# Performance work log

Measured on AMD Instinct MI355X. Metric: run time of the kernel, lower is better.

The kernel has to match this reference:

```python
import jax, jax.numpy as jnp
import numpy as np

B, N, D = 16, 256, 1152
HR = 1.0
H = int(N * HR)              # token-mixer hidden dim = 256
TOP_K = int(3 * D**2 / (2 * HR * N**2 + 10 * D))  # = 27
TOP_K = max(1, TOP_K)
E = 10 * TOP_K               # 270 experts
MLP_H = int(D * 4.0)


def gelu_tanh(x):
    return jax.nn.gelu(x, approximate=True)


def setup_inputs() -> dict:
    key = jax.random.key(0)
    ks = jax.random.split(key, 16)
    s = 0.02
    return {
        "x": jax.random.normal(ks[0], (B, N, D), jnp.float32),
        "c": jax.random.normal(ks[1], (B, D), jnp.float32),
        "router_w": jax.random.normal(ks[2], (E, D), jnp.float32) * s,
        "fc1_w": jax.random.normal(ks[3], (E, H, N), jnp.float32) * s,
        "fc1_b": jnp.zeros((E, H), jnp.float32),
        "fc2_w": jax.random.normal(ks[4], (E, N, H), jnp.float32) * s,
        "fc2_b": jnp.zeros((E, N), jnp.float32),
        "out_proj_w": jax.random.normal(ks[5], (D, D), jnp.float32) * s,
        "out_proj_b": jnp.zeros((D,), jnp.float32),
        "adaln_w": jax.random.normal(ks[6], (6 * D, D), jnp.float32) * s,
        "adaln_b": jnp.zeros((6 * D,), jnp.float32),
        "mlp_w1": jax.random.normal(ks[7], (MLP_H, D), jnp.float32) * s,
        "mlp_b1": jnp.zeros((MLP_H,), jnp.float32),
        "mlp_w2": jax.random.normal(ks[8], (D, MLP_H), jnp.float32) * s,
        "mlp_b2": jnp.zeros((D,), jnp.float32),
    }


def _forward(x, c, router_w, fc1_w, fc1_b, fc2_w, fc2_b,
             out_proj_w, out_proj_b, adaln_w, adaln_b,
             mlp_w1, mlp_b1, mlp_w2, mlp_b2):
    # adaLN modulation: SiLU -> Linear(D, 6D) -> chunk 6
    mod = jax.nn.silu(c) @ adaln_w.T + adaln_b                      # [B, 6D]
    sh_mom, sc_mom, g_mom, sh_mlp, sc_mlp, g_mlp = jnp.split(mod, 6, axis=1)
    modx = x * (1.0 + sc_mom[:, None, :]) + sh_mom[:, None, :]      # [B,N,D]

    # ---- Mixture of Mixers ----
    router_logits = modx.mean(axis=1) @ router_w.T                  # [B,E]
    probs = jax.nn.softmax(router_logits, axis=-1)
    topk_w, topk_idx = jax.lax.top_k(probs, TOP_K)                  # [B,K]
    topk_w = topk_w / topk_w.sum(axis=-1, keepdims=True)

    # TokenMixer layernorm: normalize across token axis (dim=1), eps 1e-5, no affine
    mu = modx.mean(axis=1, keepdims=True)
    var = modx.var(axis=1, keepdims=True)
    z = (modx - mu) * jax.lax.rsqrt(var + 1e-5)                     # [B,N,D]

    # Gather selected expert weights and apply token-mixing MLP per slot
    w1 = fc1_w[topk_idx]                                            # [B,K,H,N]
    b1 = fc1_b[topk_idx]                                            # [B,K,H]
    w2 = fc2_w[topk_idx]                                            # [B,K,N,H]
    b2 = fc2_b[topk_idx]                                            # [B,K,N]
    h = jnp.einsum('bkhn,bnd->bkhd', w1, z) + b1[..., None]         # [B,K,H,D]
    h = gelu_tanh(h)
    o = jnp.einsum('bknh,bkhd->bknd', w2, h) + b2[..., None]        # [B,K,N,D]
    mom = jnp.einsum('bk,bknd->bnd', topk_w, o)                     # [B,N,D]
    mom_out = mom @ out_proj_w.T + out_proj_b

    # load-balancing aux loss (top-1 routing fraction)
    top1 = topk_idx[:, 0]
    frac = jax.nn.one_hot(top1, E, dtype=probs.dtype).mean(axis=0)  # [E]
    aux_loss = E * jnp.sum(probs.mean(axis=0) * frac)

    x = x + g_mom[:, None, :] * mom_out

    # norm2: LN over last dim, eps 1e-6, no affine
    mu2 = x.mean(axis=-1, keepdims=True)
    var2 = x.var(axis=-1, keepdims=True)
    n2 = (x - mu2) * jax.lax.rsqrt(var2 + 1e-6)
    m = n2 * (1.0 + sc_mlp[:, None, :]) + sh_mlp[:, None, :]
    mlp = gelu_tanh(m @ mlp_w1.T + mlp_b1) @ mlp_w2.T + mlp_b2
    x = x + g_mlp[:, None, :] * mlp
    return x, aux_loss


def reference(x, c, router_w, fc1_w, fc1_b, fc2_w, fc2_b,
              out_proj_w, out_proj_b, adaln_w, adaln_b,
              mlp_w1, mlp_b1, mlp_w2, mlp_b2):
    return _forward(x, c, router_w, fc1_w, fc1_b, fc2_w, fc2_b,
                    out_proj_w, out_proj_b, adaln_w, adaln_b,
                    mlp_w1, mlp_b1, mlp_w2, mlp_b2)
```

## Files before the change

kernel.cpp:

```cpp
#include <hip/hip_runtime.h>
#include <stdint.h>


#define B_ 16
#define N_ 256
#define D_ 1152
#define E_ 270
#define KTOP 27
#define MLPH 4608
#define D6 6912

typedef float f32;
typedef unsigned short u16;
typedef unsigned int u32;

typedef __attribute__((ext_vector_type(8))) short bf16x8;
typedef __attribute__((ext_vector_type(4))) float f32x4;

__device__ __forceinline__ u16 f2b(f32 x){
  union{f32 f;u32 u;} v; v.f=x;
  u32 r=v.u+0x7FFFu+((v.u>>16)&1u);
  return (u16)(r>>16);
}
__device__ __forceinline__ u32 f2b2(f32 a,f32 b){ return (u32)f2b(a)|((u32)f2b(b)<<16); }
__device__ __forceinline__ f32 gelu_t(f32 x){
  f32 u=0.7978845608028654f*(x+0.044715f*x*x*x);
  f32 e=__expf(2.0f*u);
  return 0.5f*x*(2.0f-2.0f/(e+1.0f));
}
__device__ __forceinline__ f32x4 mfma16(bf16x8 a,bf16x8 b,f32x4 c){
  return __builtin_amdgcn_mfma_f32_16x16x32_bf16(a,b,c,0,0,0);
}

__global__ void k_modinit(f32* __restrict__ mod, const f32* __restrict__ adb){
  int i=blockIdx.x*256+threadIdx.x;
  mod[i]=adb[i%D6];
}
__global__ void k_adaln(f32* __restrict__ mod, const f32* __restrict__ c, const f32* __restrict__ aw){
  __shared__ f32 scs[B_][128];
  const int tid=threadIdx.x;
  const int d0=blockIdx.y*128;
  for(int i=tid;i<B_*128;i+=256){
    int b=i>>7,d=i&127;
    f32 v=c[b*D_+d0+d];
    scs[b][d]=v/(1.f+__expf(-v));
  }
  __syncthreads();
  const int j=blockIdx.x*256+tid;
  f32 acc[B_];
  #pragma unroll
  for(int b=0;b<B_;b++) acc[b]=0.f;
  const f32* wr=aw+(size_t)j*D_+d0;
  for(int d=0;d<128;d+=4){
    float4 w4=*(const float4*)(wr+d);
    #pragma unroll
    for(int b=0;b<B_;b++)
      acc[b]+=w4.x*scs[b][d]+w4.y*scs[b][d+1]+w4.z*scs[b][d+2]+w4.w*scs[b][d+3];
  }
  #pragma unroll
  for(int b=0;b<B_;b++) atomicAdd(&mod[b*D6+j],acc[b]);
}

__global__ void k_colstats(f32* __restrict__ mu, f32* __restrict__ rstd,
                           const f32* __restrict__ x, const f32* __restrict__ mod){
  const int d=(blockIdx.x*64+threadIdx.x)*2;
  const int b=blockIdx.y;
  const f32* xp=x+(size_t)b*N_*D_+d;
  f32 s1a=0,s1b=0,s2a=0,s2b=0;
  for(int n=0;n<N_;n++){
    float2 v=*(const float2*)(xp+(size_t)n*D_);
    s1a+=v.x; s1b+=v.y; s2a+=v.x*v.x; s2b+=v.y*v.y;
  }
  #pragma unroll
  for(int q=0;q<2;q++){
    f32 s1=q?s1b:s1a, s2=q?s2b:s2a;
    int dd=d+q;
    f32 xb=s1*(1.f/N_);
    f32 vx=s2*(1.f/N_)-xb*xb;
    f32 a=1.f+mod[b*D6+D_+dd];
    f32 m=xb*a+mod[b*D6+dd];
    mu[b*D_+dd]=m;
    rstd[b*D_+dd]=rsqrtf(vx*a*a+1e-5f);
  }
}

__global__ void k_ztrans(u16* __restrict__ zt, const f32* __restrict__ x,
                         const f32* __restrict__ mu, const f32* __restrict__ rstd,
                         const f32* __restrict__ mod){
  __shared__ f32 xs[64][129];
  const int tid=threadIdx.x;
  const int dt0=blockIdx.x*128, n0=blockIdx.y*64, b=blockIdx.z;
  const f32* xp=x+((size_t)b*N_+n0)*D_+dt0;
  for(int s=tid;s<2048;s+=256){
    int n=s>>5, cq=(s&31)*4;
    float4 v=*(const float4*)(xp+(size_t)n*D_+cq);
    xs[n][cq]=v.x; xs[n][cq+1]=v.y; xs[n][cq+2]=v.z; xs[n][cq+3]=v.w;
  }
  __syncthreads();
  for(int s=tid;s<1024;s+=256){
    int d=s>>3, g=s&7;
    int gd=dt0+d;
    f32 a=1.f+mod[b*D6+D_+gd];
    f32 sh=mod[b*D6+gd];
    f32 m=mu[b*D_+gd], rs=rstd[b*D_+gd];
    f32 z[8];
    #pragma unroll
    for(int i=0;i<8;i++) z[i]=(xs[g*8+i][d]*a+sh-m)*rs;
    uint4 o; o.x=f2b2(z[0],z[1]); o.y=f2b2(z[2],z[3]); o.z=f2b2(z[4],z[5]); o.w=f2b2(z[6],z[7]);
    *(uint4*)(zt+((size_t)b*D_+gd)*N_+n0+g*8)=o;
  }
}

__global__ void k_router(f32* __restrict__ logits, const f32* __restrict__ mu, const f32* __restrict__ rw){
  const int e=blockIdx.x, lane=threadIdx.x;
  f32 acc[B_];
  #pragma unroll
  for(int b=0;b<B_;b++) acc[b]=0.f;
  const f32* wr=rw+(size_t)e*D_;
  for(int i=0;i<9;i++){
    const int d=(lane+i*64)*2;
    const float2 w2=*(const float2*)(wr+d);
    #pragma unroll
    for(int b=0;b<B_;b++){
      const float2 m2=*(const float2*)(mu+b*D_+d);
      acc[b]+=w2.x*m2.x+w2.y*m2.y;
    }
  }
  #pragma unroll
  for(int b=0;b<B_;b++){
    f32 v=acc[b];
    #pragma unroll
    for(int off=32;off;off>>=1) v+=__shfl_xor(v,off);
    if(lane==0) logits[b*E_+e]=v;
  }
}

__global__ void k_topk(int* __restrict__ tki, f32* __restrict__ tkw, f32* __restrict__ bias_n,
                       f32* __restrict__ aux_out, const f32* __restrict__ logits,
                       const f32* __restrict__ b2){
  __shared__ f32 probs[B_][E_];
  __shared__ int top1[B_];
  const int tid=threadIdx.x, b=tid>>6, lane=tid&63;
  f32 p[5];
  f32 mx=-1e30f;
  #pragma unroll
  for(int i=0;i<5;i++){ int e=lane+i*64; p[i]=(e<E_)?logits[b*E_+e]:-1e30f; mx=fmaxf(mx,p[i]); }
  #pragma unroll
  for(int off=32;off;off>>=1) mx=fmaxf(mx,__shfl_xor(mx,off));
  f32 sum=0;
  #pragma unroll
  for(int i=0;i<5;i++){ int e=lane+i*64; if(e<E_){ p[i]=__expf(p[i]-mx); sum+=p[i]; } else p[i]=-1.f; }
  #pragma unroll
  for(int off=32;off;off>>=1) sum+=__shfl_xor(sum,off);
  const f32 inv=1.f/sum;
  #pragma unroll
  for(int i=0;i<5;i++){ int e=lane+i*64; if(e<E_){ p[i]*=inv; probs[b][e]=p[i]; } }
  int sidx[KTOP]; f32 sp[KTOP]; f32 swsum=0;
  for(int k=0;k<KTOP;k++){
    f32 bv=-2.f; int bi=E_;
    #pragma unroll
    for(int i=0;i<5;i++){ int e=lane+i*64; if(p[i]>bv||(p[i]==bv&&e<bi)){bv=p[i];bi=e;} }
    #pragma unroll
    for(int off=32;off;off>>=1){
      f32 ov=__shfl_xor(bv,off); int oi=__shfl_xor(bi,off);
      if(ov>bv||(ov==bv&&oi<bi)){bv=ov;bi=oi;}
    }
    sidx[k]=bi; sp[k]=bv; swsum+=bv;
    #pragma unroll
    for(int i=0;i<5;i++){ int e=lane+i*64; if(e==bi) p[i]=-1.f; }
  }
  if(lane==0){
    top1[b]=sidx[0];
    for(int k=0;k<KTOP;k++){ tki[b*KTOP+k]=sidx[k]; tkw[b*KTOP+k]=sp[k]/swsum; }
  }
  f32 accn[4]={0,0,0,0};
  for(int k=0;k<KTOP;k++){
    const f32* br=b2+(size_t)sidx[k]*N_;
    const f32 w=sp[k]/swsum;
    #pragma unroll
    for(int j=0;j<4;j++) accn[j]+=w*br[lane+j*64];
  }
  #pragma unroll
  for(int j=0;j<4;j++) bias_n[b*N_+lane+j*64]=accn[j];
  __syncthreads();
  if(tid<64){
    f32 s=0;
    for(int pr=tid;pr<256;pr+=64) s+=probs[pr&15][top1[pr>>4]];
    #pragma unroll
    for(int off=32;off;off>>=1) s+=__shfl_xor(s,off);
    if(tid==0) aux_out[0]=s*((f32)E_/(f32)(B_*B_));
  }
}

__global__ void k_wconv(u16* __restrict__ dst, const f32* __restrict__ src){
  const size_t i=((size_t)blockIdx.x*256+threadIdx.x)*8;
  float4 a=*(const float4*)(src+i), b4=*(const float4*)(src+i+4);
  uint4 o; o.x=f2b2(a.x,a.y); o.y=f2b2(a.z,a.w); o.z=f2b2(b4.x,b4.y); o.w=f2b2(b4.z,b4.w);
  *(uint4*)(dst+i)=o;
}

__global__ __launch_bounds__(512,2) void k_expert(
  f32* __restrict__ mom, const u16* __restrict__ w1b, const u16* __restrict__ w2b,
  const u16* __restrict__ zt, const int* __restrict__ tki, const f32* __restrict__ tkw,
  const f32* __restrict__ fc1b){
  __shared__ u16 wc[2][256][40];
  __shared__ u16 zc[2][128][40];
  __shared__ u16 hlds[128][264];
  __shared__ f32 b1s[256];
  const int tid=threadIdx.x, lane=tid&63, wave=tid>>6;
  const int dt0=blockIdx.x*128, b=blockIdx.z, k0=blockIdx.y*9;
  const int row0=wave*32, c16=lane&15, r4=((lane>>4)<<2), kof=((lane>>4)<<3);
  const int wr0=tid>>2, wq=tid&3;
  const int zr=tid>>2, zq=tid&3;
  f32x4 macc[2][8];
  #pragma unroll
  for(int i=0;i<2;i++)
    #pragma unroll
    for(int j=0;j<8;j++) macc[i][j]=(f32x4){0.f,0.f,0.f,0.f};
  const u16* ztb=zt+((size_t)b*D_+dt0)*N_;
  uint4 rw0,rw1,rz;
  for(int kk=0;kk<9;kk++){
    const int e=tki[b*KTOP+k0+kk];
    const f32 wk=tkw[b*KTOP+k0+kk];
    const u16* W1=w1b+(size_t)e*65536;
    const u16* W2=w2b+(size_t)e*65536;
    if(tid<256) b1s[tid]=fc1b[e*256+tid];
    f32x4 hacc[2][8];
    #pragma unroll
    for(int i=0;i<2;i++)
      #pragma unroll
      for(int j=0;j<8;j++) hacc[i][j]=(f32x4){0.f,0.f,0.f,0.f};
    rw0=*(const uint4*)(W1+(size_t)wr0*256+wq*8);
    rw1=*(const uint4*)(W1+(size_t)(wr0+128)*256+wq*8);
    rz =*(const uint4*)(ztb+(size_t)zr*256+zq*8);
    *(uint4*)&wc[0][wr0][wq*8]=rw0;
    *(uint4*)&wc[0][wr0+128][wq*8]=rw1;
    *(uint4*)&zc[0][zr][zq*8]=rz;
    __syncthreads();
    #pragma unroll 1
    for(int kc=0;kc<8;kc++){
      if(kc<7){
        rw0=*(const uint4*)(W1+(size_t)wr0*256+(kc+1)*32+wq*8);
        rw1=*(const uint4*)(W1+(size_t)(wr0+128)*256+(kc+1)*32+wq*8);
        rz =*(const uint4*)(ztb+(size_t)zr*256+(kc+1)*32+zq*8);
      }
      {
        const int bi=kc&1;
        bf16x8 af0=*(const bf16x8*)&wc[bi][row0+c16][kof];
        bf16x8 af1=*(const bf16x8*)&wc[bi][row0+16+c16][kof];
        #pragma unroll
        for(int ct=0;ct<8;ct++){
          bf16x8 bfr=*(const bf16x8*)&zc[bi][ct*16+c16][kof];
          hacc[0][ct]=mfma16(af0,bfr,hacc[0][ct]);
          hacc[1][ct]=mfma16(af1,bfr,hacc[1][ct]);
        }
      }
      if(kc<7){
        const int bi=(kc+1)&1;
        *(uint4*)&wc[bi][wr0][wq*8]=rw0;
        *(uint4*)&wc[bi][wr0+128][wq*8]=rw1;
        *(uint4*)&zc[bi][zr][zq*8]=rz;
      }
      __syncthreads();
    }
    #pragma unroll
    for(int rt=0;rt<2;rt++){
      const int hr=row0+rt*16+r4;
      #pragma unroll
      for(int ct=0;ct<8;ct++){
        const int dcol=ct*16+c16;
        f32 v0=gelu_t(hacc[rt][ct][0]+b1s[hr+0])*wk;
        f32 v1=gelu_t(hacc[rt][ct][1]+b1s[hr+1])*wk;
        f32 v2=gelu_t(hacc[rt][ct][2]+b1s[hr+2])*wk;
        f32 v3=gelu_t(hacc[rt][ct][3]+b1s[hr+3])*wk;
        uint2 o; o.x=f2b2(v0,v1); o.y=f2b2(v2,v3);
        *(uint2*)&hlds[dcol][hr]=o;
      }
    }
    rw0=*(const uint4*)(W2+(size_t)wr0*256+wq*8);
    rw1=*(const uint4*)(W2+(size_t)(wr0+128)*256+wq*8);
    *(uint4*)&wc[0][wr0][wq*8]=rw0;
    *(uint4*)&wc[0][wr0+128][wq*8]=rw1;
    __syncthreads();
    #pragma unroll 1
    for(int kc=0;kc<8;kc++){
      if(kc<7){
        rw0=*(const uint4*)(W2+(size_t)wr0*256+(kc+1)*32+wq*8);
        rw1=*(const uint4*)(W2+(size_t)(wr0+128)*256+(kc+1)*32+wq*8);
      }
      {
        const int bi=kc&1;
        bf16x8 af0=*(const bf16x8*)&wc[bi][row0+c16][kof];
        bf16x8 af1=*(const bf16x8*)&wc[bi][row0+16+c16][kof];
        #pragma unroll
        for(int ct=0;ct<8;ct++){
          bf16x8 bfr=*(const bf16x8*)&hlds[ct*16+c16][kc*32+kof];
          macc[0][ct]=mfma16(af0,bfr,macc[0][ct]);
          macc[1][ct]=mfma16(af1,bfr,macc[1][ct]);
        }
      }
      if(kc<7){
        const int bi=(kc+1)&1;
        *(uint4*)&wc[bi][wr0][wq*8]=rw0;
        *(uint4*)&wc[bi][wr0+128][wq*8]=rw1;
      }
      __syncthreads();
    }
  }
  f32* mb=mom+(size_t)b*N_*D_+dt0;
  #pragma unroll
  for(int rt=0;rt<2;rt++){
    const int nr=row0+rt*16+r4;
    #pragma unroll
    for(int ct=0;ct<8;ct++){
      const int dc=ct*16+c16;
      #pragma unroll
      for(int j=0;j<4;j++)
        atomicAdd(&mb[(size_t)(nr+j)*D_+dc],macc[rt][ct][j]);
    }
  }
}

__global__ void k_momcomb(u16* __restrict__ mb, const f32* __restrict__ mom, const f32* __restrict__ bias_n){
  const size_t i=((size_t)blockIdx.x*256+threadIdx.x)*4;
  const int t=(int)(i/D_);
  float4 a=*(const float4*)(mom+i);
  const f32 bn=bias_n[t];
  uint2 o; o.x=f2b2(a.x+bn,a.y+bn); o.y=f2b2(a.z+bn,a.w+bn);
  *(uint2*)(mb+i)=o;
}

template<int EPI>
__global__ __launch_bounds__(256,2) void k_gemm(
  const u16* __restrict__ A, const f32* __restrict__ Wf, const f32* __restrict__ bias,
  const f32* __restrict__ aux1, const f32* __restrict__ mod,
  f32* __restrict__ outf, u16* __restrict__ outb, const int K, const int ldo){
  __shared__ u16 asb[2][128][72];
  __shared__ u16 wsb[2][128][72];
  const int tid=threadIdx.x, lane=tid&63, wave=tid>>6;
  const int nt0=blockIdx.x*128, mt0=blockIdx.y*128;
  const int row0=wave*32, c16=lane&15, r4=((lane>>4)<<2), kof=((lane>>4)<<3);
  f32x4 acc[2][8];
  #pragma unroll
  for(int i=0;i<2;i++)
    #pragma unroll
    for(int j=0;j<8;j++) acc[i][j]=(f32x4){0.f,0.f,0.f,0.f};
  const int NK=K>>6;
  uint4 ra[4]; float4 rwv[8];
  auto ldA=[&](int kc){
    #pragma unroll
    for(int s=0;s<4;s++){ int slot=tid+s*256; int row=slot>>3,q=slot&7;
      ra[s]=*(const uint4*)(A+(size_t)(mt0+row)*K+(size_t)kc*64+q*8); } };
  auto stA=[&](int bi){
    #pragma unroll
    for(int s=0;s<4;s++){ int slot=tid+s*256; int row=slot>>3,q=slot&7;
      *(uint4*)&asb[bi][row][q*8]=ra[s]; } };
  auto ldW=[&](int kc){
    #pragma unroll
    for(int s=0;s<4;s++){ int slot=tid+s*256; int row=slot>>3,q=slot&7;
      const f32* p=Wf+(size_t)(nt0+row)*K+(size_t)kc*64+q*8;
      rwv[2*s]=*(const float4*)p; rwv[2*s+1]=*(const float4*)(p+4); } };
  auto stW=[&](int bi){
    #pragma unroll
    for(int s=0;s<4;s++){ int slot=tid+s*256; int row=slot>>3,q=slot&7;
      uint4 o; o.x=f2b2(rwv[2*s].x,rwv[2*s].y); o.y=f2b2(rwv[2*s].z,rwv[2*s].w);
      o.z=f2b2(rwv[2*s+1].x,rwv[2*s+1].y); o.w=f2b2(rwv[2*s+1].z,rwv[2*s+1].w);
      *(uint4*)&wsb[bi][row][q*8]=o; } };
  ldA(0); ldW(0); stA(0); stW(0);
  __syncthreads();
  #pragma unroll 1
  for(int kc=0;kc<NK;kc++){
    if(kc+1<NK){ ldA(kc+1); ldW(kc+1); }
    {
      const int bi=kc&1;
      #pragma unroll
      for(int ks=0;ks<2;ks++){
        bf16x8 af0=*(const bf16x8*)&asb[bi][row0+c16][ks*32+kof];
        bf16x8 af1=*(const bf16x8*)&asb[bi][row0+16+c16][ks*32+kof];
        #pragma unroll
        for(int ct=0;ct<8;ct++){
          bf16x8 bfr=*(const bf16x8*)&wsb[bi][ct*16+c16][ks*32+kof];
          acc[0][ct]=mfma16(af0,bfr,acc[0][ct]);
          acc[1][ct]=mfma16(af1,bfr,acc[1][ct]);
        }
      }
    }
    if(kc+1<NK){ stA((kc+1)&1); stW((kc+1)&1); }
    __syncthreads();
  }
  #pragma unroll
  for(int rt=0;rt<2;rt++){
    #pragma unroll
    for(int ct=0;ct<8;ct++){
      const int cc=nt0+ct*16+c16;
      const f32 bv=bias[cc];
      #pragma unroll
      for(int j=0;j<4;j++){
        const int r=mt0+row0+rt*16+r4+j;
        f32 v=acc[rt][ct][j]+bv;
        if constexpr(EPI==1){
          f32 g=mod[(r>>8)*D6+2*D_+cc];
          outf[(size_t)r*ldo+cc]=aux1[(size_t)r*ldo+cc]+g*v;
        } else if constexpr(EPI==2){
          outb[(size_t)r*ldo+cc]=f2b(gelu_t(v));
        } else {
          f32 g=mod[(r>>8)*D6+5*D_+cc];
          outf[(size_t)r*ldo+cc]=aux1[(size_t)r*D_+cc]+g*v;
        }
      }
    }
  }
}

__global__ void k_ln2(f32* __restrict__ st, const f32* __restrict__ y){
  const int t=blockIdx.x, tid=threadIdx.x;
  f32 s1=0,s2=0;
  for(int i=tid;i<D_;i+=128){ f32 v=y[(size_t)t*D_+i]; s1+=v; s2+=v*v; }
  #pragma unroll
  for(int off=32;off;off>>=1){ s1+=__shfl_xor(s1,off); s2+=__shfl_xor(s2,off); }
  __shared__ f32 r1[2],r2[2];
  if((tid&63)==0){ r1[tid>>6]=s1; r2[tid>>6]=s2; }
  __syncthreads();
  if(tid==0){
    f32 a=r1[0]+r1[1], q=r2[0]+r2[1];
    f32 m=a*(1.0f/D_);
    f32 var=q*(1.0f/D_)-m*m;
    st[t*2]=m; st[t*2+1]=rsqrtf(var+1e-6f);
  }
}

__global__ void k_mnorm(u16* __restrict__ mb, const f32* __restrict__ y,
                        const f32* __restrict__ st, const f32* __restrict__ mod){
  const size_t i=((size_t)blockIdx.x*256+threadIdx.x)*4;
  const int t=(int)(i/D_); const int b=t>>8; const int d=(int)(i-(size_t)t*D_);
  float4 v=*(const float4*)(y+i);
  const f32 m=st[t*2], rs=st[t*2+1];
  float4 sc=*(const float4*)(mod+b*D6+4*D_+d);
  float4 sh=*(const float4*)(mod+b*D6+3*D_+d);
  f32 a0=(v.x-m)*rs*(1.f+sc.x)+sh.x;
  f32 a1=(v.y-m)*rs*(1.f+sc.y)+sh.y;
  f32 a2=(v.z-m)*rs*(1.f+sc.z)+sh.z;
  f32 a3=(v.w-m)*rs*(1.f+sc.w)+sh.w;
  uint2 o; o.x=f2b2(a0,a1); o.y=f2b2(a2,a3);
  *(uint2*)(mb+i)=o;
}

extern "C" void kernel_launch(void* const* d_in, const int* in_sizes, int n_in,
                              void* d_out, int out_size, void* d_ws, size_t ws_size,
                              hipStream_t stream){
  const f32* x  =(const f32*)d_in[0];
  const f32* c  =(const f32*)d_in[1];
  const f32* rw =(const f32*)d_in[2];
  const f32* f1w=(const f32*)d_in[3];
  const f32* f1b=(const f32*)d_in[4];
  const f32* f2w=(const f32*)d_in[5];
  const f32* f2b_=(const f32*)d_in[6];
  const f32* opw=(const f32*)d_in[7];
  const f32* opb=(const f32*)d_in[8];
  const f32* adw=(const f32*)d_in[9];
  const f32* adb=(const f32*)d_in[10];
  const f32* m1w=(const f32*)d_in[11];
  const f32* m1b=(const f32*)d_in[12];
  const f32* m2w=(const f32*)d_in[13];
  const f32* m2b=(const f32*)d_in[14];
  f32* out=(f32*)d_out;

  char* wsp=(char*)d_ws; size_t off=0;
  auto alloc=[&](size_t bytes)->void*{ void* p=wsp+off; off=(off+bytes+255)&~(size_t)255; return p; };
  f32* mod   =(f32*)alloc((size_t)B_*D6*4);
  f32* mu    =(f32*)alloc((size_t)B_*D_*4);
  f32* rstd  =(f32*)alloc((size_t)B_*D_*4);
  f32* logits=(f32*)alloc((size_t)B_*E_*4);
  int* tki   =(int*)alloc((size_t)B_*KTOP*4);
  f32* tkw   =(f32*)alloc((size_t)B_*KTOP*4);
  f32* bias_n=(f32*)alloc((size_t)B_*N_*4);
  f32* ln2st =(f32*)alloc((size_t)B_*N_*2*4);
  u16* mom_b =(u16*)alloc((size_t)B_*N_*D_*2);
  u16* zt    =(u16*)alloc((size_t)B_*N_*D_*2);
  u16* w1b   =(u16*)alloc((size_t)E_*65536*2);
  u16* w2b   =(u16*)alloc((size_t)E_*65536*2);
  f32* mom=out;
  f32* y  =out;
  u16* m_b=zt;
  u16* t_b=w1b;
  f32* aux_out=out+(size_t)B_*N_*D_;

  hipMemsetAsync(mom,0,(size_t)B_*N_*D_*4,stream);
  k_modinit<<<432,256,0,stream>>>(mod,adb);
  k_adaln<<<dim3(27,9),256,0,stream>>>(mod,c,adw);
  k_colstats<<<dim3(9,16),64,0,stream>>>(mu,rstd,x,mod);
  k_ztrans<<<dim3(9,4,16),256,0,stream>>>(zt,x,mu,rstd,mod);
  k_router<<<E_,64,0,stream>>>(logits,mu,rw);
  k_topk<<<1,1024,0,stream>>>(tki,tkw,bias_n,aux_out,logits,f2b_);
  k_wconv<<<8640,256,0,stream>>>(w1b,f1w);
  k_wconv<<<8640,256,0,stream>>>(w2b,f2w);
  k_expert<<<dim3(9,3,16),512,0,stream>>>(mom,w1b,w2b,zt,tki,tkw,f1b);
  k_momcomb<<<4608,256,0,stream>>>(mom_b,mom,bias_n);
  k_gemm<1><<<dim3(9,32),256,0,stream>>>(mom_b,opw,opb,x,mod,y,nullptr,D_,D_);
  k_ln2<<<4096,128,0,stream>>>(ln2st,y);
  k_mnorm<<<4608,256,0,stream>>>(m_b,y,ln2st,mod);
  k_gemm<2><<<dim3(36,32),256,0,stream>>>(m_b,m1w,m1b,nullptr,nullptr,nullptr,t_b,D_,MLPH);
  k_gemm<3><<<dim3(9,32),256,0,stream>>>(t_b,m2w,m2b,y,mod,out,nullptr,MLPH,D_);
}
```

Baseline: 1.127 ms.

## Retile expert kernel, pre-convert dense weights to bf16, add grid swizzle

The expert kernel is restructured to split the hidden dimension into two 128-row halves. fc1 and fc2 now run as two smaller GEMM stages that reuse the z tile's LDS for the hidden activations. Smaller LDS lets occupancy rise to 4 blocks, and the grid is flattened with an 8-way swizzle. The dense GEMMs now read bf16 weights that are pre-converted once by extra k_wconv launches, instead of converting fp32 in the inner loop. They also gain an M-tile template (64 rows for the D-output GEMMs) and the same block swizzle. The trade-offs are extra conversion passes and more synchronisation points in the expert kernel.

New measurement: 1.579 ms. +40.1%, slower.

```diff
diff --git a/kernel.cpp b/kernel.cpp
--- a/kernel.cpp
+++ b/kernel.cpp
@@ -105,7 +105,7 @@
     f32 m=mu[b*D_+gd], rs=rstd[b*D_+gd];
     f32 z[8];
     #pragma unroll
-    for(int i=0;i<8;i++) z[i]=(xs[g*8+i][d]*a+sh-m)*rs;
+    for(int i2=0;i2<8;i2++) z[i2]=(xs[g*8+i2][d]*a+sh-m)*rs;
     uint4 o; o.x=f2b2(z[0],z[1]); o.y=f2b2(z[2],z[3]); o.z=f2b2(z[4],z[5]); o.w=f2b2(z[6],z[7]);
     *(uint4*)(zt+((size_t)b*D_+gd)*N_+n0+g*8)=o;
   }
@@ -199,124 +199,121 @@
   *(uint4*)(dst+i)=o;
 }
 
-__global__ __launch_bounds__(512,2) void k_expert(
+__global__ __launch_bounds__(512,4) void k_expert(
   f32* __restrict__ mom, const u16* __restrict__ w1b, const u16* __restrict__ w2b,
   const u16* __restrict__ zt, const int* __restrict__ tki, const f32* __restrict__ tkw,
   const f32* __restrict__ fc1b){
-  __shared__ u16 wc[2][256][40];
-  __shared__ u16 zc[2][128][40];
-  __shared__ u16 hlds[128][264];
+  __shared__ __align__(16) u16 wc[2][128][72];
+  __shared__ __align__(16) u16 zc[2][128][72];
   __shared__ f32 b1s[256];
+  u16 (*hlds)[136]=reinterpret_cast<u16 (*)[136]>(&zc[0][0][0]);
+  const int bid=blockIdx.x;
+  const int g8=bid&7, jj=bid>>3;
+  const int xb=jj%9, ghi=jj/9;
+  const int g=ghi*8+g8;
+  const int b=g/3, ks=g%3;
+  const int dt0=xb*128;
   const int tid=threadIdx.x, lane=tid&63, wave=tid>>6;
-  const int dt0=blockIdx.x*128, b=blockIdx.z, k0=blockIdx.y*9;
-  const int row0=wave*32, c16=lane&15, r4=((lane>>4)<<2), kof=((lane>>4)<<3);
-  const int wr0=tid>>2, wq=tid&3;
-  const int zr=tid>>2, zq=tid&3;
-  f32x4 macc[2][8];
+  const int c16=lane&15, r4=(lane>>4)<<2, kof=(lane>>4)<<3;
+  const int srow=tid>>2, sq=(tid&3)<<4;
+  f32x4 acc2[2][8];
   #pragma unroll
   for(int i=0;i<2;i++)
     #pragma unroll
-    for(int j=0;j<8;j++) macc[i][j]=(f32x4){0.f,0.f,0.f,0.f};
+    for(int j=0;j<8;j++) acc2[i][j]=(f32x4){0.f,0.f,0.f,0.f};
   const u16* ztb=zt+((size_t)b*D_+dt0)*N_;
-  uint4 rw0,rw1,rz;
   for(int kk=0;kk<9;kk++){
-    const int e=tki[b*KTOP+k0+kk];
-    const f32 wk=tkw[b*KTOP+k0+kk];
-    const u16* W1=w1b+(size_t)e*65536;
-    const u16* W2=w2b+(size_t)e*65536;
+    const int e=tki[b*KTOP+ks*9+kk];
+    const f32 wk=tkw[b*KTOP+ks*9+kk];
     if(tid<256) b1s[tid]=fc1b[e*256+tid];
-    f32x4 hacc[2][8];
-    #pragma unroll
-    for(int i=0;i<2;i++)
+    uint4 a0,a1,z0,z1;
+    #pragma unroll 1
+    for(int hh=0;hh<2;hh++){
+      const u16* W1h=w1b+(size_t)e*65536+hh*128*256;
+      f32x4 acc1[8];
       #pragma unroll
-      for(int j=0;j<8;j++) hacc[i][j]=(f32x4){0.f,0.f,0.f,0.f};
-    rw0=*(const uint4*)(W1+(size_t)wr0*256+wq*8);
-    rw1=*(const uint4*)(W1+(size_t)(wr0+128)*256+wq*8);
-    rz =*(const uint4*)(ztb+(size_t)zr*256+zq*8);
-    *(uint4*)&wc[0][wr0][wq*8]=rw0;
-    *(uint4*)&wc[0][wr0+128][wq*8]=rw1;
-    *(uint4*)&zc[0][zr][zq*8]=rz;
-    __syncthreads();
-    #pragma unroll 1
-    for(int kc=0;kc<8;kc++){
-      if(kc<7){
-        rw0=*(const uint4*)(W1+(size_t)wr0*256+(kc+1)*32+wq*8);
-        rw1=*(const uint4*)(W1+(size_t)(wr0+128)*256+(kc+1)*32+wq*8);
-        rz =*(const uint4*)(ztb+(size_t)zr*256+(kc+1)*32+zq*8);
+      for(int j=0;j<8;j++) acc1[j]=(f32x4){0.f,0.f,0.f,0.f};
+      a0=*(const uint4*)(W1h+srow*256+sq);   a1=*(const uint4*)(W1h+srow*256+sq+8);
+      z0=*(const uint4*)(ztb+(size_t)srow*256+sq); z1=*(const uint4*)(ztb+(size_t)srow*256+sq+8);
+      *(uint4*)&wc[0][srow][sq]=a0; *(uint4*)&wc[0][srow][sq+8]=a1;
+      *(uint4*)&zc[0][srow][sq]=z0; *(uint4*)&zc[0][srow][sq+8]=z1;
+      __syncthreads();
+      #pragma unroll 1
+      for(int kc=0;kc<4;kc++){
+        if(kc<3){
+          const int co=(kc+1)*64+sq;
+          a0=*(const uint4*)(W1h+srow*256+co);   a1=*(const uint4*)(W1h+srow*256+co+8);
+          z0=*(const uint4*)(ztb+(size_t)srow*256+co); z1=*(const uint4*)(ztb+(size_t)srow*256+co+8);
+        }
+        const int bi=kc&1;
+        #pragma unroll
+        for(int k2=0;k2<2;k2++){
+          bf16x8 af=*(const bf16x8*)&wc[bi][wave*16+c16][k2*32+kof];
+          #pragma unroll
+          for(int ct=0;ct<8;ct++){
+            bf16x8 bf=*(const bf16x8*)&zc[bi][ct*16+c16][k2*32+kof];
+            acc1[ct]=mfma16(af,bf,acc1[ct]);
+          }
+        }
+        if(kc<3){
+          const int nb=(kc+1)&1;
+          *(uint4*)&wc[nb][srow][sq]=a0; *(uint4*)&wc[nb][srow][sq+8]=a1;
+          *(uint4*)&zc[nb][srow][sq]=z0; *(uint4*)&zc[nb][srow][sq+8]=z1;
+        }
+        __syncthreads();
       }
-      {
-        const int bi=kc&1;
-        bf16x8 af0=*(const bf16x8*)&wc[bi][row0+c16][kof];
-        bf16x8 af1=*(const bf16x8*)&wc[bi][row0+16+c16][kof];
-        #pragma unroll
-        for(int ct=0;ct<8;ct++){
-          bf16x8 bfr=*(const bf16x8*)&zc[bi][ct*16+c16][kof];
-          hacc[0][ct]=mfma16(af0,bfr,hacc[0][ct]);
-          hacc[1][ct]=mfma16(af1,bfr,hacc[1][ct]);
+      f32 bb[4];
+      #pragma unroll
+      for(int j=0;j<4;j++) bb[j]=b1s[hh*128+wave*16+r4+j];
+      #pragma unroll
+      for(int ct=0;ct<8;ct++){
+        f32 v0=gelu_t(acc1[ct][0]+bb[0])*wk;
+        f32 v1=gelu_t(acc1[ct][1]+bb[1])*wk;
+        f32 v2=gelu_t(acc1[ct][2]+bb[2])*wk;
+        f32 v3=gelu_t(acc1[ct][3]+bb[3])*wk;
+        uint2 o; o.x=f2b2(v0,v1); o.y=f2b2(v2,v3);
+        *(uint2*)&hlds[ct*16+c16][wave*16+r4]=o;
+      }
+      __syncthreads();
+      #pragma unroll 1
+      for(int nh=0;nh<2;nh++){
+        const u16* W2h=w2b+(size_t)e*65536+nh*128*256+hh*128;
+        a0=*(const uint4*)(W2h+srow*256+sq); a1=*(const uint4*)(W2h+srow*256+sq+8);
+        *(uint4*)&wc[0][srow][sq]=a0; *(uint4*)&wc[0][srow][sq+8]=a1;
+        __syncthreads();
+        #pragma unroll 1
+        for(int kc=0;kc<2;kc++){
+          if(kc<1){
+            a0=*(const uint4*)(W2h+srow*256+64+sq); a1=*(const uint4*)(W2h+srow*256+64+sq+8);
+          }
+          const int bi=kc&1;
+          #pragma unroll
+          for(int k2=0;k2<2;k2++){
+            bf16x8 af=*(const bf16x8*)&wc[bi][wave*16+c16][k2*32+kof];
+            #pragma unroll
+            for(int ct=0;ct<8;ct++){
+              bf16x8 bf=*(const bf16x8*)&hlds[ct*16+c16][kc*64+k2*32+kof];
+              acc2[nh][ct]=mfma16(af,bf,acc2[nh][ct]);
+            }
+          }
+          if(kc<1){
+            *(uint4*)&wc[1][srow][sq]=a0; *(uint4*)&wc[1][srow][sq+8]=a1;
+          }
+          __syncthreads();
         }
       }
-      if(kc<7){
-        const int bi=(kc+1)&1;
-        *(uint4*)&wc[bi][wr0][wq*8]=rw0;
-        *(uint4*)&wc[bi][wr0+128][wq*8]=rw1;
-        *(uint4*)&zc[bi][zr][zq*8]=rz;
-      }
-      __syncthreads();
     }
-    #pragma unroll
-    for(int rt=0;rt<2;rt++){
-      const int hr=row0+rt*16+r4;
-      #pragma unroll
-      for(int ct=0;ct<8;ct++){
-        const int dcol=ct*16+c16;
-        f32 v0=gelu_t(hacc[rt][ct][0]+b1s[hr+0])*wk;
-        f32 v1=gelu_t(hacc[rt][ct][1]+b1s[hr+1])*wk;
-        f32 v2=gelu_t(hacc[rt][ct][2]+b1s[hr+2])*wk;
-        f32 v3=gelu_t(hacc[rt][ct][3]+b1s[hr+3])*wk;
-        uint2 o; o.x=f2b2(v0,v1); o.y=f2b2(v2,v3);
-        *(uint2*)&hlds[dcol][hr]=o;
-      }
-    }
-    rw0=*(const uint4*)(W2+(size_t)wr0*256+wq*8);
-    rw1=*(const uint4*)(W2+(size_t)(wr0+128)*256+wq*8);
-    *(uint4*)&wc[0][wr0][wq*8]=rw0;
-    *(uint4*)&wc[0][wr0+128][wq*8]=rw1;
-    __syncthreads();
-    #pragma unroll 1
-    for(int kc=0;kc<8;kc++){
-      if(kc<7){
-        rw0=*(const uint4*)(W2+(size_t)wr0*256+(kc+1)*32+wq*8);
-        rw1=*(const uint4*)(W2+(size_t)(wr0+128)*256+(kc+1)*32+wq*8);
-      }
-      {
-        const int bi=kc&1;
-        bf16x8 af0=*(const bf16x8*)&wc[bi][row0+c16][kof];
-        bf16x8 af1=*(const bf16x8*)&wc[bi][row0+16+c16][kof];
-        #pragma unroll
-        for(int ct=0;ct<8;ct++){
-          bf16x8 bfr=*(const bf16x8*)&hlds[ct*16+c16][kc*32+kof];
-          macc[0][ct]=mfma16(af0,bfr,macc[0][ct]);
-          macc[1][ct]=mfma16(af1,bfr,macc[1][ct]);
-        }
-      }
-      if(kc<7){
-        const int bi=(kc+1)&1;
-        *(uint4*)&wc[bi][wr0][wq*8]=rw0;
-        *(uint4*)&wc[bi][wr0+128][wq*8]=rw1;
-      }
-      __syncthreads();
-    }
   }
   f32* mb=mom+(size_t)b*N_*D_+dt0;
   #pragma unroll
-  for(int rt=0;rt<2;rt++){
-    const int nr=row0+rt*16+r4;
+  for(int nh=0;nh<2;nh++){
+    const int nr=nh*128+wave*16+r4;
     #pragma unroll
     for(int ct=0;ct<8;ct++){
       const int dc=ct*16+c16;
       #pragma unroll
       for(int j=0;j<4;j++)
-        atomicAdd(&mb[(size_t)(nr+j)*D_+dc],macc[rt][ct][j]);
+        atomicAdd(&mb[(size_t)(nr+j)*D_+dc],acc2[nh][ct][j]);
     }
   }
 }
@@ -330,42 +327,45 @@
   *(uint2*)(mb+i)=o;
 }
 
-template<int EPI>
+template<int MT,int EPI>
 __global__ __launch_bounds__(256,2) void k_gemm(
-  const u16* __restrict__ A, const f32* __restrict__ Wf, const f32* __restrict__ bias,
+  const u16* __restrict__ A, const u16* __restrict__ W, const f32* __restrict__ bias,
   const f32* __restrict__ aux1, const f32* __restrict__ mod,
   f32* __restrict__ outf, u16* __restrict__ outb, const int K, const int ldo){
-  __shared__ u16 asb[2][128][72];
-  __shared__ u16 wsb[2][128][72];
+  constexpr int RT=MT/64;
+  constexpr int AN=MT/32;
+  __shared__ __align__(16) u16 asb[2][MT][72];
+  __shared__ __align__(16) u16 wsb[2][128][72];
+  const int lin=blockIdx.x+gridDim.x*blockIdx.y;
+  const int y8=lin&7, t2=lin>>3;
+  const int xb=t2%gridDim.x, yhi=t2/gridDim.x;
+  const int yb=yhi*8+y8;
+  const int nt0=xb*128, mt0=yb*MT;
   const int tid=threadIdx.x, lane=tid&63, wave=tid>>6;
-  const int nt0=blockIdx.x*128, mt0=blockIdx.y*128;
-  const int row0=wave*32, c16=lane&15, r4=((lane>>4)<<2), kof=((lane>>4)<<3);
-  f32x4 acc[2][8];
-  #pragma unroll
-  for(int i=0;i<2;i++)
+  const int c16=lane&15, r4=(lane>>4)<<2, kof=(lane>>4)<<3;
+  const int row0=wave*16*RT;
+  const int wrow=tid>>1, wq=(tid&1)<<5;
+  const int arow=(MT==128)?(tid>>1):(tid>>2);
+  const int aq  =(MT==128)?((tid&1)<<5):((tid&3)<<4);
+  f32x4 acc[RT][8];
+  #pragma unroll
+  for(int i=0;i<RT;i++)
     #pragma unroll
     for(int j=0;j<8;j++) acc[i][j]=(f32x4){0.f,0.f,0.f,0.f};
   const int NK=K>>6;
-  uint4 ra[4]; float4 rwv[8];
+  uint4 ra[AN], rw[4];
   auto ldA=[&](int kc){
     #pragma unroll
-    for(int s=0;s<4;s++){ int slot=tid+s*256; int row=slot>>3,q=slot&7;
-      ra[s]=*(const uint4*)(A+(size_t)(mt0+row)*K+(size_t)kc*64+q*8); } };
+    for(int s=0;s<AN;s++) ra[s]=*(const uint4*)(A+(size_t)(mt0+arow)*K+kc*64+aq+s*8); };
   auto stA=[&](int bi){
     #pragma unroll
-    for(int s=0;s<4;s++){ int slot=tid+s*256; int row=slot>>3,q=slot&7;
-      *(uint4*)&asb[bi][row][q*8]=ra[s]; } };
+    for(int s=0;s<AN;s++) *(uint4*)&asb[bi][arow][aq+s*8]=ra[s]; };
   auto ldW=[&](int kc){
     #pragma unroll
-    for(int s=0;s<4;s++){ int slot=tid+s*256; int row=slot>>3,q=slot&7;
-      const f32* p=Wf+(size_t)(nt0+row)*K+(size_t)kc*64+q*8;
-      rwv[2*s]=*(const float4*)p; rwv[2*s+1]=*(const float4*)(p+4); } };
+    for(int s=0;s<4;s++) rw[s]=*(const uint4*)(W+(size_t)(nt0+wrow)*K+kc*64+wq+s*8); };
   auto stW=[&](int bi){
     #pragma unroll
-    for(int s=0;s<4;s++){ int slot=tid+s*256; int row=slot>>3,q=slot&7;
-      uint4 o; o.x=f2b2(rwv[2*s].x,rwv[2*s].y); o.y=f2b2(rwv[2*s].z,rwv[2*s].w);
-      o.z=f2b2(rwv[2*s+1].x,rwv[2*s+1].y); o.w=f2b2(rwv[2*s+1].z,rwv[2*s+1].w);
-      *(uint4*)&wsb[bi][row][q*8]=o; } };
+    for(int s=0;s<4;s++) *(uint4*)&wsb[bi][wrow][wq+s*8]=rw[s]; };
   ldA(0); ldW(0); stA(0); stW(0);
   __syncthreads();
   #pragma unroll 1
@@ -374,14 +374,15 @@
     {
       const int bi=kc&1;
       #pragma unroll
-      for(int ks=0;ks<2;ks++){
-        bf16x8 af0=*(const bf16x8*)&asb[bi][row0+c16][ks*32+kof];
-        bf16x8 af1=*(const bf16x8*)&asb[bi][row0+16+c16][ks*32+kof];
+      for(int k2=0;k2<2;k2++){
         #pragma unroll
-        for(int ct=0;ct<8;ct++){
-          bf16x8 bfr=*(const bf16x8*)&wsb[bi][ct*16+c16][ks*32+kof];
-          acc[0][ct]=mfma16(af0,bfr,acc[0][ct]);
-          acc[1][ct]=mfma16(af1,bfr,acc[1][ct]);
+        for(int rt=0;rt<RT;rt++){
+          bf16x8 af=*(const bf16x8*)&asb[bi][row0+rt*16+c16][k2*32+kof];
+          #pragma unroll
+          for(int ct=0;ct<8;ct++){
+            bf16x8 bf=*(const bf16x8*)&wsb[bi][ct*16+c16][k2*32+kof];
+            acc[rt][ct]=mfma16(af,bf,acc[rt][ct]);
+          }
         }
       }
     }
@@ -389,7 +390,7 @@
     __syncthreads();
   }
   #pragma unroll
-  for(int rt=0;rt<2;rt++){
+  for(int rt=0;rt<RT;rt++){
     #pragma unroll
     for(int ct=0;ct<8;ct++){
       const int cc=nt0+ct*16+c16;
@@ -399,13 +400,13 @@
         const int r=mt0+row0+rt*16+r4+j;
         f32 v=acc[rt][ct][j]+bv;
         if constexpr(EPI==1){
-          f32 g=mod[(r>>8)*D6+2*D_+cc];
-          outf[(size_t)r*ldo+cc]=aux1[(size_t)r*ldo+cc]+g*v;
+          f32 gmod=mod[(r>>8)*D6+2*D_+cc];
+          outf[(size_t)r*ldo+cc]=aux1[(size_t)r*ldo+cc]+gmod*v;
         } else if constexpr(EPI==2){
           outb[(size_t)r*ldo+cc]=f2b(gelu_t(v));
         } else {
-          f32 g=mod[(r>>8)*D6+5*D_+cc];
-          outf[(size_t)r*ldo+cc]=aux1[(size_t)r*D_+cc]+g*v;
+          f32 gmod=mod[(r>>8)*D6+5*D_+cc];
+          outf[(size_t)r*ldo+cc]=aux1[(size_t)r*ldo+cc]+gmod*v;
         }
       }
     }
@@ -483,6 +484,9 @@
   f32* y  =out;
   u16* m_b=zt;
   u16* t_b=w1b;
+  u16* opwb=w1b+(size_t)18874368;
+  u16* m1wb=opwb+(size_t)1327104;
+  u16* m2wb=m1wb+(size_t)5308416;
   f32* aux_out=out+(size_t)B_*N_*D_;
 
   hipMemsetAsync(mom,0,(size_t)B_*N_*D_*4,stream);
@@ -494,11 +498,14 @@
   k_topk<<<1,1024,0,stream>>>(tki,tkw,bias_n,aux_out,logits,f2b_);
   k_wconv<<<8640,256,0,stream>>>(w1b,f1w);
   k_wconv<<<8640,256,0,stream>>>(w2b,f2w);
-  k_expert<<<dim3(9,3,16),512,0,stream>>>(mom,w1b,w2b,zt,tki,tkw,f1b);
+  k_expert<<<432,512,0,stream>>>(mom,w1b,w2b,zt,tki,tkw,f1b);
+  k_wconv<<<648,256,0,stream>>>(opwb,opw);
+  k_wconv<<<2592,256,0,stream>>>(m1wb,m1w);
+  k_wconv<<<2592,256,0,stream>>>(m2wb,m2w);
   k_momcomb<<<4608,256,0,stream>>>(mom_b,mom,bias_n);
-  k_gemm<1><<<dim3(9,32),256,0,stream>>>(mom_b,opw,opb,x,mod,y,nullptr,D_,D_);
+  k_gemm<64,1><<<dim3(9,64),256,0,stream>>>(mom_b,opwb,opb,x,mod,y,nullptr,D_,D_);
   k_ln2<<<4096,128,0,stream>>>(ln2st,y);
   k_mnorm<<<4608,256,0,stream>>>(m_b,y,ln2st,mod);
-  k_gemm<2><<<dim3(36,32),256,0,stream>>>(m_b,m1w,m1b,nullptr,nullptr,nullptr,t_b,D_,MLPH);
-  k_gemm<3><<<dim3(9,32),256,0,stream>>>(t_b,m2w,m2b,y,mod,out,nullptr,MLPH,D_);
-}
+  k_gemm<128,2><<<dim3(36,32),256,0,stream>>>(m_b,m1wb,m1b,nullptr,nullptr,nullptr,t_b,D_,MLPH);
+  k_gemm<64,3><<<dim3(9,64),256,0,stream>>>(t_b,m2wb,m2b,y,mod,out,nullptr,MLPH,D_);
+}
```
